# Kernel tuning notes

Measured on AMD Instinct MI355X. Metric: run time of the kernel, lower is better.

Reference implementation:

```python
import jax, jax.numpy as jnp
import numpy as np

DIM = 256
CTX_DIM = 768
GROUPS = 8
EPS = 1e-5


def setup_inputs() -> dict:
    key = jax.random.key(0)
    ks = jax.random.split(key, 16)
    B, C, H, W, L = 16, DIM, 64, 64, 77
    s_conv = 1.0 / np.sqrt(C * 9)
    s_q = 1.0 / np.sqrt(C)
    s_kv = 1.0 / np.sqrt(CTX_DIM)
    return {
        "x": jax.random.normal(ks[0], (B, C, H, W), jnp.float32),
        "context": jax.random.normal(ks[1], (B, L, CTX_DIM), jnp.float32),
        "conv_w": jax.random.uniform(ks[2], (C, C, 3, 3), jnp.float32, -s_conv, s_conv),
        "conv_b": jax.random.uniform(ks[3], (C,), jnp.float32, -s_conv, s_conv),
        "gn_w": jnp.ones((C,), jnp.float32),
        "gn_b": jnp.zeros((C,), jnp.float32),
        "wq": jax.random.uniform(ks[4], (C, C), jnp.float32, -s_q, s_q),
        "bq": jax.random.uniform(ks[5], (C,), jnp.float32, -s_q, s_q),
        "wk": jax.random.uniform(ks[6], (C, CTX_DIM), jnp.float32, -s_kv, s_kv),
        "bk": jax.random.uniform(ks[7], (C,), jnp.float32, -s_kv, s_kv),
        "wv": jax.random.uniform(ks[8], (C, CTX_DIM), jnp.float32, -s_kv, s_kv),
        "bv": jax.random.uniform(ks[9], (C,), jnp.float32, -s_kv, s_kv),
        "wo": jax.random.uniform(ks[10], (C, C), jnp.float32, -s_q, s_q),
        "bo": jax.random.uniform(ks[11], (C,), jnp.float32, -s_q, s_q),
    }


def _group_norm(h, gn_w, gn_b):
    B, C, H, W = h.shape
    g = h.reshape(B, GROUPS, C // GROUPS, H, W)
    mean = g.mean(axis=(2, 3, 4), keepdims=True)
    var = g.var(axis=(2, 3, 4), keepdims=True)
    g = (g - mean) * jax.lax.rsqrt(var + EPS)
    h = g.reshape(B, C, H, W)
    return h * gn_w[None, :, None, None] + gn_b[None, :, None, None]


def reference(x, context, conv_w, conv_b, gn_w, gn_b, wq, bq, wk, bk, wv, bv, wo, bo):
    B, C, H, W = x.shape
    # conv 3x3, padding=1 (NCHW, OIHW)
    h = jax.lax.conv_general_dilated(
        x, conv_w, window_strides=(1, 1), padding=((1, 1), (1, 1)),
        dimension_numbers=("NCHW", "OIHW", "NCHW"))
    h = h + conv_b[None, :, None, None]
    h = jax.nn.silu(_group_norm(h, gn_w, gn_b))
    # flatten spatial -> tokens: [B, HW, C]
    hf = h.reshape(B, C, H * W).transpose(0, 2, 1)
    q = hf @ wq.T + bq                     # [B, HW, C]
    k = context @ wk.T + bk                # [B, L, C]
    v = context @ wv.T + bv                # [B, L, C]
    scale = 1.0 / jnp.sqrt(jnp.asarray(C, q.dtype))
    att = jax.nn.softmax(jnp.einsum("bqc,bkc->bqk", q, k) * scale, axis=-1)
    o = jnp.einsum("bqk,bkc->bqc", att, v) @ wo.T + bo
    h_att = o.transpose(0, 2, 1).reshape(B, C, H, W)
    return x + h_att
```

## Files before the change

### kernel.cpp

```cpp
#include <hip/hip_runtime.h>
#include <stdint.h>

#define B_  16
#define C_  256
#define HW_ 4096
#define Hp  66
#define PP  4356
#define EPS_ 1e-5f

typedef unsigned short u16;
typedef unsigned int   u32;
typedef __attribute__((ext_vector_type(4))) float  f32x4;
typedef __attribute__((ext_vector_type(8))) __bf16 bf16x8;
typedef __attribute__((ext_vector_type(8))) u16    u16x8;

__device__ __forceinline__ float bf2f(u16 u){ u32 x = ((u32)u)<<16; float f; __builtin_memcpy(&f,&x,4); return f; }
__device__ __forceinline__ u16 f2bf(float f){ u32 x; __builtin_memcpy(&x,&f,4); u32 r = x + 0x7fffu + ((x>>16)&1u); return (u16)(r>>16); }

__device__ __forceinline__ void g2l16(const void* g, void* l){
  __builtin_amdgcn_global_load_lds((__attribute__((address_space(1))) void*)(void*)g,
                                   (__attribute__((address_space(3))) void*)l, 16, 0, 0);
}
__device__ __forceinline__ bf16x8 ldfrag(const u16* p){
  u16x8 r = *(const u16x8*)p;
  return __builtin_bit_cast(bf16x8, r);
}

__global__ __launch_bounds__(256) void k_prep(const float* __restrict__ x, u16* __restrict__ xpT,
    const float* __restrict__ conv_w, const float* __restrict__ wq, const float* __restrict__ wo,
    const float* __restrict__ wk, const float* __restrict__ wv, const float* __restrict__ ctx,
    u16* __restrict__ wBt, u16* __restrict__ wqB, u16* __restrict__ woB,
    u16* __restrict__ wkvB, u16* __restrict__ ctxB, float* __restrict__ stats){
  __shared__ float Lt[64*65];
  int bid = blockIdx.x; int tid = threadIdx.x;
  if(bid >= 1056){
    int i = (bid-1056)*256 + tid;
    if(i < 589824){
      int j = i&7, co = (i>>3)&255, atom = (i>>11)&3, g = i>>13;
      int t = g%9, cic = g/9;
      int ciF = cic*32 + atom*8 + j;
      wBt[i] = f2bf(conv_w[(co*256+ciF)*9 + t]); return;
    }
    i -= 589824;
    if(i < 65536){ wqB[i] = f2bf(wq[i]); return; } i -= 65536;
    if(i < 65536){ woB[i] = f2bf(wo[i]); return; } i -= 65536;
    if(i < 196608){ wkvB[i] = f2bf(wk[i]); return; } i -= 196608;
    if(i < 196608){ wkvB[196608+i] = f2bf(wv[i]); return; } i -= 196608;
    if(i < 946176){ ctxB[i] = f2bf(ctx[i]); return; } i -= 946176;
    if(i < 512){ stats[i] = 0.f; }
    return;
  }
  int b = bid/66, hh = bid - b*66;
  if(hh==0 || hh==65){
    for(int i=tid;i<32*264;i+=256){
      int pl = i/264, off = i - pl*264;
      u32* p = (u32*)(xpT + ((size_t)(b*32+pl)*PP + (size_t)hh*Hp)*8);
      p[off] = 0u;
    }
    return;
  }
  {
    int pl = tid>>3, q = tid&7;
    size_t base = ((size_t)(b*32+pl)*PP + (size_t)hh*Hp + (q>=4?65:0))*8;
    ((u32*)(xpT + base))[q&3] = 0u;
  }
  int h = hh-1;
  for(int cc=0; cc<4; cc++){
    int c0=cc*64;
    int ci = tid>>2, w0 = (tid&3)*16;
    const float* xs = x + ((size_t)(b*C_ + c0+ci)*HW_) + h*64 + w0;
    for(int j=0;j<4;j++){
      float4 v = *(const float4*)(xs + j*4);
      Lt[ci*65 + w0 + j*4 + 0] = v.x;
      Lt[ci*65 + w0 + j*4 + 1] = v.y;
      Lt[ci*65 + w0 + j*4 + 2] = v.z;
      Lt[ci*65 + w0 + j*4 + 3] = v.w;
    }
    __syncthreads();
    int w = tid>>2, cj = (tid&3)*16;
    union { u16 u[16]; uint4 v[2]; } outu;
    for(int j=0;j<16;j++) outu.u[j] = f2bf(Lt[(cj+j)*65 + w]);
    int chan = c0 + cj;
    int cic = chan>>5, at0 = (chan>>3)&3;
    u16* dst = xpT + (((size_t)(b*8+cic)*4 + at0)*PP + (size_t)hh*Hp + w + 1)*8;
    *(uint4*)dst = outu.v[0];
    *(uint4*)(dst + (size_t)PP*8) = outu.v[1];
    __syncthreads();
  }
}

__global__ __launch_bounds__(256, 3) void k_conv(const u16* __restrict__ xpT, const u16* __restrict__ wBt,
    const float* __restrict__ conv_b, u16* __restrict__ h, float* __restrict__ stats){
  __shared__ u16 As[2][264*32];
  __shared__ u16 Bs[2][128*32];
  int bid0 = blockIdx.x;
  int l = (bid0 & 7)*128 + (bid0 >> 3);
  int b = l >> 6, hp = (l >> 1) & 31, nh = l & 1;
  int tid = threadIdx.x;
  int w = tid>>6, lane = tid&63, ln = lane&15, qd = lane>>4;
  int wm = w&1, wn = w>>1;
  f32x4 acc[4][4] = {};
  int hr_[4], wp_[4];
  #pragma unroll
  for(int mf=0;mf<4;mf++){ int p = wm*64 + mf*16 + ln; hr_[mf] = p>>6; wp_[mf] = p&63; }

  #pragma unroll
  for(int r=0;r<5;r++){
    int c = r*256 + tid;
    if(c < 1056){
      int atom = c/264, ipix = c - atom*264;
      g2l16(xpT + (((size_t)(b*8+0)*4 + atom)*PP + hp*132 + ipix)*8, &As[0][c*8]);
    }
  }
  #pragma unroll
  for(int r=0;r<2;r++){
    int c = r*256 + tid;
    int atom = c>>7, col = c&127;
    g2l16(wBt + ((size_t)atom*2048 + (nh*128+col)*8), &Bs[0][c*8]);
  }
  __syncthreads();

  int cb = 0;
  for(int ci=0; ci<8; ci++){
    int ca = ci&1;
    for(int t=0;t<9;t++){
      int tn = t+1, cin = ci;
      if(tn==9){ tn=0; cin=ci+1; }
      if(cin < 8){
        #pragma unroll
        for(int r=0;r<2;r++){
          int c = r*256 + tid;
          int atom = c>>7, col = c&127;
          g2l16(wBt + (((size_t)(cin*9+tn)*4 + atom)*2048 + (nh*128+col)*8), &Bs[cb^1][c*8]);
        }
      }
      if(t<5 && ci<7){
        int c = t*256 + tid;
        if(c < 1056){
          int atom = c/264, ipix = c - atom*264;
          g2l16(xpT + (((size_t)(b*8+ci+1)*4 + atom)*PP + hp*132 + ipix)*8, &As[ca^1][c*8]);
        }
      }
      int dy = (t*11)>>5, dx = t - dy*3;
      bf16x8 af[4], bfv[4];
      #pragma unroll
      for(int mf=0;mf<4;mf++){
        int ipix = (hr_[mf]+dy)*66 + wp_[mf] + dx;
        af[mf] = ldfrag(&As[ca][(qd*264 + ipix)*8]);
      }
      #pragma unroll
      for(int nf=0;nf<4;nf++) bfv[nf] = ldfrag(&Bs[cb][(qd*128 + wn*64+nf*16+ln)*8]);
      #pragma unroll
      for(int mf=0;mf<4;mf++)
        #pragma unroll
        for(int nf=0;nf<4;nf++)
          acc[mf][nf] = __builtin_amdgcn_mfma_f32_16x16x32_bf16(af[mf], bfv[nf], acc[mf][nf], 0,0,0);
      __syncthreads();
      cb ^= 1;
    }
  }
  float s[2]={0,0}, q[2]={0,0};
  int p0 = hp*128;
  for(int nf=0;nf<4;nf++){
    int n = nh*128 + wn*64 + nf*16 + ln;
    float bias = conv_b[n];
    for(int mf=0;mf<4;mf++){
      for(int r=0;r<4;r++){
        int p = wm*64 + mf*16 + qd*4 + r;
        float v = acc[mf][nf][r] + bias;
        h[((size_t)(b*HW_ + p0 + p))*C_ + n] = f2bf(v);
        s[nf>>1]+=v; q[nf>>1]+=v*v;
      }
    }
  }
  for(int off=32;off>=1;off>>=1){
    #pragma unroll
    for(int g=0;g<2;g++){ s[g]+=__shfl_down(s[g],off,64); q[g]+=__shfl_down(q[g],off,64); }
  }
  if(lane==0){
    #pragma unroll
    for(int g=0;g<2;g++){
      int gg = nh*4 + wn*2 + g;
      atomicAdd(&stats[(b*8 + gg)*2+0], s[g]);
      atomicAdd(&stats[(b*8 + gg)*2+1], q[g]);
    }
  }
}

__global__ __launch_bounds__(256, 2) void k_qgn(const u16* __restrict__ hbuf, const u16* __restrict__ wqB,
    const float* __restrict__ stats, const float* __restrict__ gnw, const float* __restrict__ gnb,
    const float* __restrict__ bq, u16* __restrict__ qb){
  __shared__ u16 As[128*32];
  __shared__ u16 Bs[256*32];
  int mt = blockIdx.x;
  int b = mt >> 5;
  int tid = threadIdx.x;
  int w = tid>>6, lane = tid&63, ln = lane&15, qd = lane>>4;
  int wm = w&1, wn = w>>1;
  int pr = tid>>1, half = tid&1;
  const u16* hsrc = hbuf + ((size_t)(mt*128+pr))*256 + half*16;
  f32x4 acc[4][8] = {};
  uint4 ra0, ra1, rb0, rb1;
  ra0 = *(const uint4*)(hsrc);
  ra1 = *(const uint4*)(hsrc + 8);
  for(int kt=0; kt<8; kt++){
    float sm = stats[(b*8+kt)*2], qm = stats[(b*8+kt)*2+1];
    float mean = sm*(1.f/131072.f);
    float rstd = rsqrtf(qm*(1.f/131072.f) - mean*mean + EPS_);
    int c0 = kt*32 + half*16;
    float4 gw0 = *(const float4*)(gnw+c0), gw1 = *(const float4*)(gnw+c0+4);
    float4 gw2 = *(const float4*)(gnw+c0+8), gw3 = *(const float4*)(gnw+c0+12);
    float4 gb0 = *(const float4*)(gnb+c0), gb1 = *(const float4*)(gnb+c0+4);
    float4 gb2 = *(const float4*)(gnb+c0+8), gb3 = *(const float4*)(gnb+c0+12);
    float gwv[16] = {gw0.x,gw0.y,gw0.z,gw0.w, gw1.x,gw1.y,gw1.z,gw1.w,
                     gw2.x,gw2.y,gw2.z,gw2.w, gw3.x,gw3.y,gw3.z,gw3.w};
    float gbv[16] = {gb0.x,gb0.y,gb0.z,gb0.w, gb1.x,gb1.y,gb1.z,gb1.w,
                     gb2.x,gb2.y,gb2.z,gb2.w, gb3.x,gb3.y,gb3.z,gb3.w};
    u16 inu[16];
    ((uint4*)inu)[0] = ra0; ((uint4*)inu)[1] = ra1;
    u16 outu[16];
    #pragma unroll
    for(int j=0;j<16;j++){
      float v = bf2f(inu[j]);
      v = (v-mean)*rstd*gwv[j] + gbv[j];
      float s = v/(1.f+__expf(-v));
      outu[j] = f2bf(s);
    }
    u16* adst = &As[pr*32 + half*16];
    ((uint4*)adst)[0] = ((uint4*)outu)[0];
    ((uint4*)adst)[1] = ((uint4*)outu)[1];
    #pragma unroll
    for(int r=0;r<4;r++){
      int c = r*256 + tid;
      int co = c>>2, atom = c&3;
      g2l16(wqB + (size_t)co*256 + kt*32 + atom*8, &Bs[c*8]);
    }
    if(kt<7){
      rb0 = *(const uint4*)(hsrc + (kt+1)*32);
      rb1 = *(const uint4*)(hsrc + (kt+1)*32 + 8);
    }
    __syncthreads();
    bf16x8 af[4], bfv[8];
    #pragma unroll
    for(int mf=0;mf<4;mf++) af[mf] = ldfrag(&As[(wm*64+mf*16+ln)*32 + qd*8]);
    #pragma unroll
    for(int nf=0;nf<8;nf++) bfv[nf] = ldfrag(&Bs[(wn*128+nf*16+ln)*32 + qd*8]);
    #pragma unroll
    for(int mf=0;mf<4;mf++)
      #pragma unroll
      for(int nf=0;nf<8;nf++)
        acc[mf][nf] = __builtin_amdgcn_mfma_f32_16x16x32_bf16(af[mf], bfv[nf], acc[mf][nf], 0,0,0);
    __syncthreads();
    ra0 = rb0; ra1 = rb1;
  }
  for(int nf=0;nf<8;nf++){
    int n = wn*128 + nf*16 + ln;
    float bias = bq[n];
    for(int mf=0;mf<4;mf++){
      for(int r=0;r<4;r++){
        int ml = wm*64 + mf*16 + qd*4 + r;
        qb[((size_t)(mt*128+ml))*256 + n] = f2bf(acc[mf][nf][r]+bias);
      }
    }
  }
}

__global__ __launch_bounds__(256) void k_kvproj(const u16* __restrict__ ctxB, const u16* __restrict__ wkvB,
    const float* __restrict__ bk, const float* __restrict__ bv,
    u16* __restrict__ kb, u16* __restrict__ vT){
  __shared__ u16 As[64*128];
  __shared__ u16 Bs[64*128];
  int bid = blockIdx.x;
  int nt = bid & 7, mt = bid >> 3;
  int n0 = nt*64, m0 = mt*64;
  int tid=threadIdx.x, w=tid>>6, lane=tid&63, ln=lane&15, qd=lane>>4;
  int wm = w&1, wn = w>>1;
  f32x4 acc[2][2]={};
  for(int kt=0;kt<6;kt++){
    #pragma unroll
    for(int r=0;r<4;r++){
      int c = r*256 + tid;
      int row = c>>4, atom = c&15;
      g2l16(ctxB + ((size_t)(m0+row)*768 + kt*128 + atom*8), &As[c*8]);
      g2l16(wkvB + ((size_t)(n0+row)*768 + kt*128 + atom*8), &Bs[c*8]);
    }
    __syncthreads();
    #pragma unroll
    for(int kk=0;kk<4;kk++){
      bf16x8 af[2], bfv[2];
      #pragma unroll
      for(int mf=0;mf<2;mf++) af[mf]=ldfrag(&As[(wm*32+mf*16+ln)*128 + kk*32 + qd*8]);
      #pragma unroll
      for(int nf=0;nf<2;nf++) bfv[nf]=ldfrag(&Bs[(wn*32+nf*16+ln)*128 + kk*32 + qd*8]);
      #pragma unroll
      for(int mf=0;mf<2;mf++)
        #pragma unroll
        for(int nf=0;nf<2;nf++)
          acc[mf][nf]=__builtin_amdgcn_mfma_f32_16x16x32_bf16(af[mf],bfv[nf],acc[mf][nf],0,0,0);
    }
    __syncthreads();
  }
  for(int mf=0;mf<2;mf++) for(int nf=0;nf<2;nf++){
    int ng = n0 + wn*32 + nf*16 + ln;
    float bias = ng<256 ? bk[ng] : bv[ng-256];
    for(int r=0;r<4;r++){
      int mg = m0 + wm*32 + mf*16 + qd*4 + r;
      if(mg<1232){
        float v=acc[mf][nf][r]+bias;
        int bb=mg/77, l=mg-bb*77;
        if(ng<256) kb[((size_t)(bb*77+l))*256+ng]=f2bf(v);
        else vT[((size_t)(bb*256+(ng-256)))*96 + l]=f2bf(v);
      }
    }
  }
}

__global__ __launch_bounds__(256, 2) void k_attn(const u16* __restrict__ qg, const u16* __restrict__ kb,
    const u16* __restrict__ vT, const u16* __restrict__ woB, const float* __restrict__ bo,
    const float* __restrict__ x, float* __restrict__ outp){
  __shared__ u16 SM[37888];
  __shared__ float invr[128];
  u16* KVf = SM;
  u16* Pb  = SM + 24576;
  u16* Ol  = SM;
  int bid=blockIdx.x; int b=bid>>5, qt=bid&31; int p0=qt*128;
  int tid=threadIdx.x, w=tid>>6, lane=tid&63, ln=lane&15, qd=lane>>4;

  #pragma unroll
  for(int j=0;j<10;j++){
    int c = tid + j*256;
    int kt = c/320, rem = c - kt*320;
    int q2 = rem/80, l = rem - q2*80;
    int ls = l<77 ? l : 76;
    g2l16(kb + ((size_t)(b*77+ls)*256 + kt*32 + q2*8), &KVf[(size_t)c*8]);
  }
  bf16x8 qf[2][8];
  #pragma unroll
  for(int mf=0;mf<2;mf++){
    const u16* qsrc = qg + ((size_t)(b*HW_ + p0 + w*32 + mf*16 + ln))*256 + qd*8;
    #pragma unroll
    for(int kt=0;kt<8;kt++) qf[mf][kt] = ldfrag(qsrc + kt*32);
  }
  __syncthreads();

  f32x4 Sa[2][5]={};
  #pragma unroll
  for(int kt=0;kt<8;kt++){
    bf16x8 kf[5];
    #pragma unroll
    for(int nf=0;nf<5;nf++) kf[nf]=ldfrag(&KVf[((size_t)kt*320 + qd*80 + nf*16+ln)*8]);
    #pragma unroll
    for(int mf=0;mf<2;mf++)
      #pragma unroll
      for(int nf=0;nf<5;nf++)
        Sa[mf][nf]=__builtin_amdgcn_mfma_f32_16x16x32_bf16(qf[mf][kt],kf[nf],Sa[mf][nf],0,0,0);
  }
  if(ln>=13){
    #pragma unroll
    for(int mf=0;mf<2;mf++)
      #pragma unroll
      for(int r=0;r<4;r++) Sa[mf][4][r] = -1e30f;
  }
  float mrow[2][4];
  #pragma unroll
  for(int mf=0;mf<2;mf++)
    #pragma unroll
    for(int r=0;r<4;r++){
      float m = Sa[mf][0][r];
      #pragma unroll
      for(int nf=1;nf<5;nf++) m = fmaxf(m, Sa[mf][nf][r]);
      mrow[mf][r]=m;
    }
  #pragma unroll
  for(int off=1;off<16;off<<=1)
    #pragma unroll
    for(int mf=0;mf<2;mf++)
      #pragma unroll
      for(int r=0;r<4;r++) mrow[mf][r] = fmaxf(mrow[mf][r], __shfl_xor(mrow[mf][r], off, 64));
  float rs[2][4]={};
  u16 pe[2][5][4];
  #pragma unroll
  for(int mf=0;mf<2;mf++)
    #pragma unroll
    for(int nf=0;nf<5;nf++)
      #pragma unroll
      for(int r=0;r<4;r++){
        float e = __expf((Sa[mf][nf][r]-mrow[mf][r])*0.0625f);
        rs[mf][r]+=e; pe[mf][nf][r]=f2bf(e);
      }
  #pragma unroll
  for(int off=1;off<16;off<<=1)
    #pragma unroll
    for(int mf=0;mf<2;mf++)
      #pragma unroll
      for(int r=0;r<4;r++) rs[mf][r] += __shfl_xor(rs[mf][r], off, 64);
  #pragma unroll
  for(int mf=0;mf<2;mf++)
    #pragma unroll
    for(int nf=0;nf<5;nf++)
      #pragma unroll
      for(int r=0;r<4;r++) Pb[(w*32+mf*16+qd*4+r)*104 + nf*16+ln] = pe[mf][nf][r];
  {
    int row = tid>>1, j0 = (tid&1)*8;
    u16x8 z = {0,0,0,0,0,0,0,0};
    *(u16x8*)&Pb[row*104 + 80 + j0] = z;
  }
  if(ln==0){
    #pragma unroll
    for(int mf=0;mf<2;mf++)
      #pragma unroll
      for(int r=0;r<4;r++) invr[w*32+mf*16+qd*4+r] = 1.f/rs[mf][r];
  }
  __syncthreads();

  #pragma unroll
  for(int j=0;j<12;j++){
    int c = tid + j*256;
    int g = c>>7, co = c&127;
    int q2 = g&3, s5 = g>>2;
    int nh2 = s5>2 ? 1 : 0, kt2 = s5 - 3*nh2;
    g2l16(vT + ((size_t)(b*256 + nh2*128 + co)*96 + kt2*32 + q2*8), &KVf[(size_t)c*8]);
  }
  __syncthreads();

  f32x4 Oa[2][2][8]={};
  #pragma unroll
  for(int nh=0;nh<2;nh++){
    #pragma unroll
    for(int kt2=0;kt2<3;kt2++){
      bf16x8 pa[2], vf[8];
      #pragma unroll
      for(int mf=0;mf<2;mf++) pa[mf]=ldfrag(&Pb[(w*32+mf*16+ln)*104 + kt2*32+qd*8]);
      #pragma unroll
      for(int nf=0;nf<8;nf++) vf[nf]=ldfrag(&KVf[(((size_t)(nh*3+kt2)*4+qd)*128 + nf*16+ln)*8]);
      #pragma unroll
      for(int mf=0;mf<2;mf++)
        #pragma unroll
        for(int nf=0;nf<8;nf++)
          Oa[nh][mf][nf]=__builtin_amdgcn_mfma_f32_16x16x32_bf16(pa[mf],vf[nf],Oa[nh][mf][nf],0,0,0);
    }
  }
  __syncthreads();

  #pragma unroll
  for(int nh=0;nh<2;nh++)
    #pragma unroll
    for(int mf=0;mf<2;mf++)
      #pragma unroll
      for(int r=0;r<4;r++){
        int ml = w*32+mf*16+qd*4+r;
        float inv = invr[ml];
        #pragma unroll
        for(int nf=0;nf<8;nf++)
          Ol[ml*264 + nh*128 + nf*16 + ln] = f2bf(Oa[nh][mf][nf][r]*inv);
      }
  __syncthreads();

  f32x4 a2[4][8] = {};
  #pragma unroll 2
  for(int kt=0;kt<8;kt++){
    bf16x8 af2[4], bf2v[8];
    #pragma unroll
    for(int mf2=0;mf2<4;mf2++)
      af2[mf2] = ldfrag(woB + (size_t)(w*64+mf2*16+ln)*256 + kt*32 + qd*8);
    #pragma unroll
    for(int nf2=0;nf2<8;nf2++)
      bf2v[nf2] = ldfrag(&Ol[(nf2*16+ln)*264 + kt*32 + qd*8]);
    #pragma unroll
    for(int mf2=0;mf2<4;mf2++)
      #pragma unroll
      for(int nf2=0;nf2<8;nf2++)
        a2[mf2][nf2] = __builtin_amdgcn_mfma_f32_16x16x32_bf16(af2[mf2], bf2v[nf2], a2[mf2][nf2],0,0,0);
  }
  #pragma unroll
  for(int mf2=0;mf2<4;mf2++)
    #pragma unroll
    for(int r=0;r<4;r++){
      int cl = w*64 + mf2*16 + qd*4 + r;
      float bias = bo[cl];
      #pragma unroll
      for(int nf2=0;nf2<8;nf2++){
        int px = p0 + nf2*16 + ln;
        size_t idx = ((size_t)(b*C_+cl))*HW_ + px;
        outp[idx] = x[idx] + a2[mf2][nf2][r] + bias;
      }
    }
}

extern "C" void kernel_launch(void* const* d_in, const int* in_sizes, int n_in,
                              void* d_out, int out_size, void* d_ws, size_t ws_size,
                              hipStream_t stream){
  const float* x      = (const float*)d_in[0];
  const float* ctx    = (const float*)d_in[1];
  const float* conv_w = (const float*)d_in[2];
  const float* conv_b = (const float*)d_in[3];
  const float* gnw    = (const float*)d_in[4];
  const float* gnb    = (const float*)d_in[5];
  const float* wq     = (const float*)d_in[6];
  const float* bq     = (const float*)d_in[7];
  const float* wk     = (const float*)d_in[8];
  const float* bk     = (const float*)d_in[9];
  const float* wv     = (const float*)d_in[10];
  const float* bv     = (const float*)d_in[11];
  const float* wo     = (const float*)d_in[12];
  const float* bo     = (const float*)d_in[13];
  char* ws = (char*)d_ws;
  u16* xpT  = (u16*)(ws + 0);
  u16* wBt  = (u16*)(ws + 35684352);
  u16* wqB  = (u16*)(ws + 36864000);
  u16* wkvB = (u16*)(ws + 36995072);
  u16* woB  = (u16*)(ws + 37781504);
  u16* ctxB = (u16*)(ws + 37912576);
  u16* hbuf = (u16*)(ws + 39804928);
  u16* kbv  = (u16*)(ws + 73359360);
  u16* vT   = (u16*)(ws + 73990144);
  float* stats = (float*)(ws + 108331008);
  u16* qb = xpT;
  float* outp = (float*)d_out;

  k_prep  <<<9106, 256, 0, stream>>>(x, xpT, conv_w, wq, wo, wk, wv, ctx, wBt, wqB, woB, wkvB, ctxB, stats);
  k_conv  <<<1024, 256, 0, stream>>>(xpT, wBt, conv_b, hbuf, stats);
  k_qgn   <<<512,  256, 0, stream>>>(hbuf, wqB, stats, gnw, gnb, bq, qb);
  k_kvproj<<<160,  256, 0, stream>>>(ctxB, wkvB, bk, bv, kbv, vT);
  k_attn  <<<512,  256, 0, stream>>>(qb, kbv, vT, woB, bo, x, outp);
}
```

Baseline: 338.8 us.

## Fuse conv, group-norm and Q projection into one cooperative kernel

Replaces the separate conv and GN+Q-projection kernels with one cooperative kernel. Each block computes a 128-pixel by 256-channel conv tile and keeps its bf16 output in LDS. It accumulates group statistics with atomics, waits at a grid-wide sync, then applies group-norm and SiLU and does the Q projection straight from LDS. This removes the global round trip of the intermediate activation and one launch, and widens the conv N tile for more reuse. The cost is a grid barrier, 512 blocks that must all be resident at once, and higher register pressure. If the cooperative launch fails, it falls back to the old two kernels.

```diff
diff --git a/kernel.cpp b/kernel.cpp
--- a/kernel.cpp
+++ b/kernel.cpp
@@ -1,5 +1,8 @@
 #include <hip/hip_runtime.h>
+#include <hip/hip_cooperative_groups.h>
 #include <stdint.h>
+
+namespace cg = cooperative_groups;
 
 #define B_  16
 #define C_  256
@@ -89,7 +92,167 @@
   }
 }
 
-__global__ __launch_bounds__(256, 3) void k_conv(const u16* __restrict__ xpT, const u16* __restrict__ wBt,
+__global__ __launch_bounds__(256, 2) void k_cgq(const u16* __restrict__ xpT, const u16* __restrict__ wBt,
+    const float* __restrict__ conv_b, float* stats,
+    const u16* __restrict__ wqB, const float* __restrict__ gnw, const float* __restrict__ gnb,
+    const float* __restrict__ bq, u16* __restrict__ qb){
+  __shared__ u16 SM[33280];
+  u16* As = SM;
+  u16* Bs = SM + 16896;
+  u16* Hl = SM;
+  int bid = blockIdx.x;
+  int b = bid >> 5, hp = bid & 31;
+  int tid = threadIdx.x;
+  int w = tid>>6, lane = tid&63, ln = lane&15, qd = lane>>4;
+  int wm = w&1, wn = w>>1;
+  f32x4 acc[4][8] = {};
+  int hr_[4], wp_[4];
+  #pragma unroll
+  for(int mf=0;mf<4;mf++){ int p = wm*64 + mf*16 + ln; hr_[mf] = p>>6; wp_[mf] = p&63; }
+
+  #pragma unroll
+  for(int r=0;r<5;r++){
+    int c = r*256 + tid;
+    if(c < 1056){
+      int atom = c/264, ipix = c - atom*264;
+      g2l16(xpT + (((size_t)(b*8+0)*4 + atom)*PP + hp*132 + ipix)*8, &As[c*8]);
+    }
+  }
+  #pragma unroll
+  for(int r=0;r<4;r++){
+    int c = r*256 + tid;
+    g2l16(wBt + (size_t)c*8, &Bs[c*8]);
+  }
+  __syncthreads();
+
+  int cb = 0;
+  for(int ci=0; ci<8; ci++){
+    int ca = ci&1;
+    for(int t=0;t<9;t++){
+      int tn = t+1, cin = ci;
+      if(tn==9){ tn=0; cin=ci+1; }
+      if(cin < 8){
+        #pragma unroll
+        for(int r=0;r<4;r++){
+          int c = r*256 + tid;
+          g2l16(wBt + ((size_t)(cin*9+tn)*8192 + c*8), &Bs[(cb^1)*8192 + c*8]);
+        }
+      }
+      if(t<5 && ci<7){
+        int c = t*256 + tid;
+        if(c < 1056){
+          int atom = c/264, ipix = c - atom*264;
+          g2l16(xpT + (((size_t)(b*8+ci+1)*4 + atom)*PP + hp*132 + ipix)*8, &As[(ca^1)*8448 + c*8]);
+        }
+      }
+      int dy = (t*11)>>5, dx = t - dy*3;
+      bf16x8 af[4], bfv[8];
+      #pragma unroll
+      for(int mf=0;mf<4;mf++){
+        int ipix = (hr_[mf]+dy)*66 + wp_[mf] + dx;
+        af[mf] = ldfrag(&As[ca*8448 + (qd*264 + ipix)*8]);
+      }
+      #pragma unroll
+      for(int nf=0;nf<8;nf++) bfv[nf] = ldfrag(&Bs[cb*8192 + (qd*256 + wn*128+nf*16+ln)*8]);
+      #pragma unroll
+      for(int mf=0;mf<4;mf++)
+        #pragma unroll
+        for(int nf=0;nf<8;nf++)
+          acc[mf][nf] = __builtin_amdgcn_mfma_f32_16x16x32_bf16(af[mf], bfv[nf], acc[mf][nf], 0,0,0);
+      __syncthreads();
+      cb ^= 1;
+    }
+  }
+
+  float s[4]={0,0,0,0}, q[4]={0,0,0,0};
+  #pragma unroll
+  for(int nf=0;nf<8;nf++){
+    int n = wn*128 + nf*16 + ln;
+    float bias = conv_b[n];
+    int oct = n>>3, sub = n&7;
+    #pragma unroll
+    for(int mf=0;mf<4;mf++){
+      #pragma unroll
+      for(int r=0;r<4;r++){
+        int p = wm*64 + mf*16 + qd*4 + r;
+        float v = acc[mf][nf][r] + bias;
+        Hl[(oct*128 + p)*8 + sub] = f2bf(v);
+        s[nf>>1]+=v; q[nf>>1]+=v*v;
+      }
+    }
+  }
+  for(int off=32;off>=1;off>>=1){
+    #pragma unroll
+    for(int g=0;g<4;g++){ s[g]+=__shfl_down(s[g],off,64); q[g]+=__shfl_down(q[g],off,64); }
+  }
+  if(lane==0){
+    #pragma unroll
+    for(int g=0;g<4;g++){
+      atomicAdd(&stats[(b*8 + wn*4 + g)*2+0], s[g]);
+      atomicAdd(&stats[(b*8 + wn*4 + g)*2+1], q[g]);
+    }
+  }
+  __threadfence();
+  cg::this_grid().sync();
+  __threadfence();
+
+  float mean_[8], rstd_[8];
+  #pragma unroll
+  for(int g=0;g<8;g++){
+    float sm = __hip_atomic_load(&stats[(b*8+g)*2+0], __ATOMIC_RELAXED, __HIP_MEMORY_SCOPE_AGENT);
+    float qm = __hip_atomic_load(&stats[(b*8+g)*2+1], __ATOMIC_RELAXED, __HIP_MEMORY_SCOPE_AGENT);
+    float mn = sm*(1.f/131072.f);
+    mean_[g] = mn;
+    rstd_[g] = rsqrtf(qm*(1.f/131072.f) - mn*mn + EPS_);
+  }
+  f32x4 a2[4][8] = {};
+  #pragma unroll
+  for(int kt=0;kt<8;kt++){
+    float mn = mean_[kt], rsd = rstd_[kt];
+    int co0 = kt*32 + qd*8;
+    float4 gw0 = *(const float4*)(gnw+co0), gw1 = *(const float4*)(gnw+co0+4);
+    float4 gb0 = *(const float4*)(gnb+co0), gb1 = *(const float4*)(gnb+co0+4);
+    float gw[8] = {gw0.x,gw0.y,gw0.z,gw0.w, gw1.x,gw1.y,gw1.z,gw1.w};
+    float gb[8] = {gb0.x,gb0.y,gb0.z,gb0.w, gb1.x,gb1.y,gb1.z,gb1.w};
+    bf16x8 af[4], bfv[8];
+    #pragma unroll
+    for(int mf=0;mf<4;mf++){
+      int row = wm*64 + mf*16 + ln;
+      u16x8 hv = *(const u16x8*)&Hl[((kt*4+qd)*128 + row)*8];
+      union { u16 u[8]; u16x8 v; } o;
+      #pragma unroll
+      for(int j=0;j<8;j++){
+        float v = bf2f(hv[j]);
+        v = (v-mn)*rsd*gw[j] + gb[j];
+        o.u[j] = f2bf(v/(1.f+__expf(-v)));
+      }
+      af[mf] = __builtin_bit_cast(bf16x8, o.v);
+    }
+    #pragma unroll
+    for(int nf=0;nf<8;nf++)
+      bfv[nf] = ldfrag(wqB + (size_t)(wn*128+nf*16+ln)*256 + kt*32 + qd*8);
+    #pragma unroll
+    for(int mf=0;mf<4;mf++)
+      #pragma unroll
+      for(int nf=0;nf<8;nf++)
+        a2[mf][nf] = __builtin_amdgcn_mfma_f32_16x16x32_bf16(af[mf], bfv[nf], a2[mf][nf], 0,0,0);
+  }
+  #pragma unroll
+  for(int nf=0;nf<8;nf++){
+    int n = wn*128 + nf*16 + ln;
+    float bias = bq[n];
+    #pragma unroll
+    for(int mf=0;mf<4;mf++){
+      #pragma unroll
+      for(int r=0;r<4;r++){
+        int ml = wm*64 + mf*16 + qd*4 + r;
+        qb[((size_t)(bid*128+ml))*256 + n] = f2bf(a2[mf][nf][r]+bias);
+      }
+    }
+  }
+}
+
+__global__ __launch_bounds__(256, 3) void k_conv_fb(const u16* __restrict__ xpT, const u16* __restrict__ wBt,
     const float* __restrict__ conv_b, u16* __restrict__ h, float* __restrict__ stats){
   __shared__ u16 As[2][264*32];
   __shared__ u16 Bs[2][128*32];
@@ -103,7 +266,6 @@
   int hr_[4], wp_[4];
   #pragma unroll
   for(int mf=0;mf<4;mf++){ int p = wm*64 + mf*16 + ln; hr_[mf] = p>>6; wp_[mf] = p&63; }
-
   #pragma unroll
   for(int r=0;r<5;r++){
     int c = r*256 + tid;
@@ -119,7 +281,6 @@
     g2l16(wBt + ((size_t)atom*2048 + (nh*128+col)*8), &Bs[0][c*8]);
   }
   __syncthreads();
-
   int cb = 0;
   for(int ci=0; ci<8; ci++){
     int ca = ci&1;
@@ -187,7 +348,7 @@
   }
 }
 
-__global__ __launch_bounds__(256, 2) void k_qgn(const u16* __restrict__ hbuf, const u16* __restrict__ wqB,
+__global__ __launch_bounds__(256, 2) void k_qgn_fb(const u16* __restrict__ hbuf, const u16* __restrict__ wqB,
     const float* __restrict__ stats, const float* __restrict__ gnw, const float* __restrict__ gnb,
     const float* __restrict__ bq, u16* __restrict__ qb){
   __shared__ u16 As[128*32];
@@ -519,8 +680,15 @@
   float* outp = (float*)d_out;
 
   k_prep  <<<9106, 256, 0, stream>>>(x, xpT, conv_w, wq, wo, wk, wv, ctx, wBt, wqB, woB, wkvB, ctxB, stats);
-  k_conv  <<<1024, 256, 0, stream>>>(xpT, wBt, conv_b, hbuf, stats);
-  k_qgn   <<<512,  256, 0, stream>>>(hbuf, wqB, stats, gnw, gnb, bq, qb);
+  {
+    void* args[] = {(void*)&xpT, (void*)&wBt, (void*)&conv_b, (void*)&stats,
+                    (void*)&wqB, (void*)&gnw, (void*)&gnb, (void*)&bq, (void*)&qb};
+    hipError_t cerr = hipLaunchCooperativeKernel((const void*)k_cgq, dim3(512), dim3(256), args, 0, stream);
+    if(cerr != hipSuccess){
+      k_conv_fb<<<1024, 256, 0, stream>>>(xpT, wBt, conv_b, hbuf, stats);
+      k_qgn_fb <<<512,  256, 0, stream>>>(hbuf, wqB, stats, gnw, gnb, bq, qb);
+    }
+  }
   k_kvproj<<<160,  256, 0, stream>>>(ctxB, wkvB, bk, bv, kbv, vT);
   k_attn  <<<512,  256, 0, stream>>>(qb, kbv, vT, woB, bo, x, outp);
 }
```

Result: slower. 493.5 us (+45.6%).
